# Kernel tuning notes

Hardware: AMD Instinct MI355X
Metric: run time of the kernel (lower is better)

The kernel has to match this reference:

```python
import jax, jax.numpy as jnp
import numpy as np

NUM_NODES = 100000
NFEAT = 128
EMBED_DIM = 128
NHEADS = 2
NHID = EMBED_DIM // NHEADS  # 64
REL_DIM = 128
NUM_REL = 500
E1 = 288000  # 1-hop edges
E2 = 32000   # 2-hop edges
E = E1 + E2
ALPHA = 0.2  # LeakyReLU slope
EPS = 1e-16


def setup_inputs() -> dict:
    key = jax.random.key(0)
    ks = jax.random.split(key, 10)
    edge_index = jax.random.randint(ks[0], (2, E), 0, NUM_NODES, dtype=jnp.int32)
    x = jax.random.normal(ks[1], (NUM_NODES, NFEAT), dtype=jnp.float32)
    r = jax.random.normal(ks[2], (NUM_REL, REL_DIM), dtype=jnp.float32)
    edge_type = jax.random.randint(ks[3], (E1,), 0, NUM_REL, dtype=jnp.int32)
    edge_type_nhop = jax.random.randint(ks[4], (E2, 2), 0, NUM_REL, dtype=jnp.int32)
    # learned params (get_param -> xavier-ish normal)
    s = 0.02
    W_heads = jax.random.normal(ks[5], (NHEADS, 2 * NFEAT + REL_DIM, NHID), dtype=jnp.float32) * s
    a_heads = jax.random.normal(ks[6], (NHEADS, NHID, 1), dtype=jnp.float32) * s
    W_out = jax.random.normal(ks[7], (2 * (NHID * NHEADS) + EMBED_DIM, NHEADS * NHID), dtype=jnp.float32) * s
    a_out = jax.random.normal(ks[8], (NHEADS * NHID, 1), dtype=jnp.float32) * s
    W_r = jax.random.normal(ks[9], (REL_DIM, EMBED_DIM), dtype=jnp.float32) * s
    return {"edge_index": edge_index, "x": x, "r": r, "edge_type": edge_type,
            "edge_type_nhop": edge_type_nhop, "W_heads": W_heads, "a_heads": a_heads,
            "W_out": W_out, "a_out": a_out, "W_r": W_r}


def _gat_layer(edge_index, x, edge_embed, W, a, concat):
    src = edge_index[0]
    dst = edge_index[1]
    # [E, 2*in + rel] -> [E, out]
    edge_h = jnp.concatenate([x[src], x[dst], edge_embed], axis=1) @ W
    e = jax.nn.leaky_relu(jnp.squeeze(edge_h @ a, axis=-1), negative_slope=ALPHA)  # [E]
    # segment softmax over src groups
    seg_max = jax.ops.segment_max(e, src, num_segments=NUM_NODES)
    w = jnp.exp(e - seg_max[src])
    denom = jax.ops.segment_sum(w, src, num_segments=NUM_NODES)
    att = w / (denom[src] + EPS)  # dropout p=0.0 -> identity
    out = jax.ops.segment_sum(att[:, None] * edge_h, src, num_segments=NUM_NODES)  # [N, out]
    return jax.nn.elu(out) if concat else out


def reference(edge_index, x, r, edge_type, edge_type_nhop, W_heads, a_heads, W_out, a_out, W_r):
    # first-pass relation edge embeddings
    edge_embed = jnp.concatenate(
        [r[edge_type], r[edge_type_nhop[:, 0]] + r[edge_type_nhop[:, 1]]], axis=0)  # [E, rel]
    # multi-head attention layers (concat heads)
    heads = [_gat_layer(edge_index, x, edge_embed, W_heads[h], a_heads[h], True)
             for h in range(NHEADS)]
    x1 = jnp.concatenate(heads, axis=1)  # [N, nheads*nhid]; dropout p=0 identity
    # transform relations
    r2 = r @ W_r  # [num_rel, embed_dim]
    edge_embed2 = jnp.concatenate(
        [r2[edge_type], r2[edge_type_nhop[:, 0]] + r2[edge_type_nhop[:, 1]]], axis=0)
    out = jax.nn.elu(_gat_layer(edge_index, x1, edge_embed2, W_out, a_out, False))
    return out, r2
```

## Files before the change

### kernel.cpp

```cpp
#include <hip/hip_runtime.h>
#include <math.h>

#define NNODES 100000
#define NREL 500
#define E1 288000
#define ETOT 320000
#define LALPHA 0.2f
#define SEPS 1e-16f
#define NB_SCAN ((NNODES + 255) / 256)
#define GTILES 6250
#define GTPB 5
#define GGRID (GTILES / GTPB)

typedef __attribute__((ext_vector_type(8))) short bf16x8;
typedef __attribute__((ext_vector_type(4))) float f32x4;

__device__ __forceinline__ unsigned short f2bf(float x) {
  unsigned int u = __float_as_uint(x);
  unsigned int r = (u + 0x7fffu + ((u >> 16) & 1u)) >> 16;
  return (unsigned short)r;
}
__device__ __forceinline__ unsigned int packbf2(float lo, float hi) {
  return (unsigned int)f2bf(lo) | ((unsigned int)f2bf(hi) << 16);
}
__device__ __forceinline__ float unpk_lo(unsigned int u) { return __uint_as_float(u << 16); }
__device__ __forceinline__ float unpk_hi(unsigned int u) {
  return __uint_as_float(u & 0xffff0000u);
}
__device__ __forceinline__ float lrelu(float e) { return (e >= 0.f) ? e : LALPHA * e; }

__device__ __forceinline__ float wave_max64(float v) {
#pragma unroll
  for (int o = 32; o >= 1; o >>= 1) v = fmaxf(v, __shfl_xor(v, o, 64));
  return v;
}
__device__ __forceinline__ float wave_sum64(float v) {
#pragma unroll
  for (int o = 32; o >= 1; o >>= 1) v += __shfl_xor(v, o, 64);
  return v;
}
__device__ __forceinline__ float red16(float v) {
  v += __shfl_xor(v, 1, 64);
  v += __shfl_xor(v, 2, 64);
  v += __shfl_xor(v, 4, 64);
  v += __shfl_xor(v, 8, 64);
  return v;
}

__global__ void k_zero_int(int* __restrict__ p, int n) {
  int i = blockIdx.x * blockDim.x + threadIdx.x;
  if (i < n) p[i] = 0;
}

__global__ void k_count(const int* __restrict__ src, int* __restrict__ cnt) {
  int e = blockIdx.x * blockDim.x + threadIdx.x;
  if (e < ETOT) atomicAdd(&cnt[src[e]], 1);
}

__global__ void k_scan_a(const int* __restrict__ cnt, int* __restrict__ rowstart,
                         int* __restrict__ blockTot) {
  __shared__ int s[256];
  int t = threadIdx.x;
  int idx = blockIdx.x * 256 + t;
  int v = (idx < NNODES) ? cnt[idx] : 0;
  s[t] = v;
  __syncthreads();
  for (int off = 1; off < 256; off <<= 1) {
    int xv = (t >= off) ? s[t - off] : 0;
    __syncthreads();
    s[t] += xv;
    __syncthreads();
  }
  if (idx < NNODES) rowstart[idx] = s[t] - v;
  if (t == 255) blockTot[blockIdx.x] = s[255];
}

__global__ void k_scan_b(const int* __restrict__ blockTot, int* __restrict__ blockOff) {
  __shared__ int s[512];
  int t = threadIdx.x;
  int v = (t < NB_SCAN) ? blockTot[t] : 0;
  s[t] = v;
  __syncthreads();
  for (int off = 1; off < 512; off <<= 1) {
    int xv = (t >= off) ? s[t - off] : 0;
    __syncthreads();
    s[t] += xv;
    __syncthreads();
  }
  if (t < NB_SCAN) blockOff[t] = s[t] - v;
}

__global__ void k_scan_c(int* __restrict__ rowstart, const int* __restrict__ blockOff,
                         int* __restrict__ cursor) {
  int idx = blockIdx.x * 256 + threadIdx.x;
  if (idx < NNODES) {
    int v = rowstart[idx] + blockOff[blockIdx.x];
    rowstart[idx] = v;
    cursor[idx] = v;
  }
  if (idx == 0) rowstart[NNODES] = ETOT;
}

__global__ void k_scatter(const int* __restrict__ src, int* __restrict__ cursor,
                          int* __restrict__ perm) {
  int e = blockIdx.x * blockDim.x + threadIdx.x;
  if (e < ETOT) {
    int pos = atomicAdd(&cursor[src[e]], 1);
    perm[pos] = e;
  }
}

__global__ void k_relprep1(const float* __restrict__ r, const float* __restrict__ Wh,
                           const float* __restrict__ ah, unsigned int* __restrict__ rW1p,
                           float* __restrict__ srel1) {
  __shared__ float vals[128];
  int t = blockIdx.x;
  int tid = threadIdx.x;
  int h = tid >> 6, kk = tid & 63;
  const float* wcol = Wh + h * 24576 + 256 * 64 + kk;
  const float* rrow = r + t * 128;
  float acc = 0.f;
#pragma unroll 4
  for (int d = 0; d < 128; ++d) acc = fmaf(rrow[d], wcol[d * 64], acc);
  vals[tid] = acc;
  float p = wave_sum64(acc * ah[h * 64 + kk]);
  if (kk == 0) srel1[t * 2 + h] = p;
  __syncthreads();
  if (tid < 64) rW1p[t * 64 + tid] = packbf2(vals[2 * tid], vals[2 * tid + 1]);
}

__global__ void k_r2(const float* __restrict__ r, const float* __restrict__ Wr,
                     float* __restrict__ r2out) {
  int t = blockIdx.x;
  int c = threadIdx.x;
  float acc = 0.f;
#pragma unroll 4
  for (int d = 0; d < 128; ++d) acc = fmaf(r[t * 128 + d], Wr[d * 128 + c], acc);
  r2out[t * 128 + c] = acc;
}

__global__ void k_relprep2(const float* __restrict__ r2, const float* __restrict__ Wo,
                           const float* __restrict__ ao, unsigned int* __restrict__ rW2p,
                           float* __restrict__ srel2) {
  __shared__ float s[128];
  __shared__ float vals[128];
  int t = blockIdx.x;
  int k = threadIdx.x;
  float acc = 0.f;
#pragma unroll 4
  for (int d = 0; d < 128; ++d) acc = fmaf(r2[t * 128 + d], Wo[(256 + d) * 128 + k], acc);
  vals[k] = acc;
  s[k] = acc * ao[k];
  __syncthreads();
  for (int off = 64; off >= 1; off >>= 1) {
    if (k < off) s[k] += s[k + off];
    __syncthreads();
  }
  if (k == 0) srel2[t] = s[0];
  if (k < 64) rW2p[t * 64 + k] = packbf2(vals[2 * k], vals[2 * k + 1]);
}

template <int LAYER>
__global__ void k_packb(const float* __restrict__ W, unsigned short* __restrict__ Wb) {
  int c = blockIdx.x;
  int d = threadIdx.x;
  float v;
  if (LAYER == 1) {
    int h = (c >> 6) & 1, part = c >> 7, kc = c & 63;
    v = W[h * 24576 + (part * 128 + d) * 64 + kc];
  } else {
    int part = c >> 7, kc = c & 127;
    v = W[(part * 128 + d) * 128 + kc];
  }
  Wb[c * 128 + d] = f2bf(v);
}

template <int LAYER>
__global__ __launch_bounds__(256) void k_gemm_mfma(const void* __restrict__ Xin,
                                                   const unsigned short* __restrict__ Wb,
                                                   const float* __restrict__ avec,
                                                   unsigned int* __restrict__ xWp,
                                                   float* __restrict__ sc) {
  const int lane = threadIdx.x & 63;
  const int wave = threadIdx.x >> 6;
  const int colv = lane & 15;
  const int kg = lane >> 4;

  bf16x8 b[4][4];
#pragma unroll
  for (int t = 0; t < 4; ++t)
#pragma unroll
    for (int s = 0; s < 4; ++s)
      b[t][s] = *(const bf16x8*)(Wb + (size_t)(wave * 64 + t * 16 + colv) * 128 + s * 32 +
                                 kg * 8);
  float av[4];
#pragma unroll
  for (int t = 0; t < 4; ++t) av[t] = avec[(wave & 1) * 64 + t * 16 + colv];
  const int slot = (LAYER == 1) ? (((wave & 1) << 1) | (wave >> 1)) : wave;

  const float4* xf4 = (const float4*)Xin;
  const uint4* xu4 = (const uint4*)Xin;
  int tile = blockIdx.x * GTPB;

  float4 cf[8];
  uint4 cu[4];
  {
    int ar = tile * 16 + colv;
    if (LAYER == 1) {
      int base = ar * 32 + kg * 2;
#pragma unroll
      for (int s = 0; s < 4; ++s) {
        cf[2 * s] = xf4[base + s * 8];
        cf[2 * s + 1] = xf4[base + s * 8 + 1];
      }
    } else {
      int base = ar * 16 + kg;
#pragma unroll
      for (int s = 0; s < 4; ++s) cu[s] = xu4[base + s * 4];
    }
  }

  for (int it = 0; it < GTPB; ++it, ++tile) {
    float4 nf[8];
    uint4 nu[4];
    const bool hasnext = (it + 1 < GTPB);
    if (hasnext) {
      int ar = (tile + 1) * 16 + colv;
      if (LAYER == 1) {
        int base = ar * 32 + kg * 2;
#pragma unroll
        for (int s = 0; s < 4; ++s) {
          nf[2 * s] = xf4[base + s * 8];
          nf[2 * s + 1] = xf4[base + s * 8 + 1];
        }
      } else {
        int base = ar * 16 + kg;
#pragma unroll
        for (int s = 0; s < 4; ++s) nu[s] = xu4[base + s * 4];
      }
    }

    bf16x8 a[4];
    if (LAYER == 1) {
#pragma unroll
      for (int s = 0; s < 4; ++s) {
        union {
          unsigned short us[8];
          bf16x8 v;
        } u;
        u.us[0] = f2bf(cf[2 * s].x); u.us[1] = f2bf(cf[2 * s].y);
        u.us[2] = f2bf(cf[2 * s].z); u.us[3] = f2bf(cf[2 * s].w);
        u.us[4] = f2bf(cf[2 * s + 1].x); u.us[5] = f2bf(cf[2 * s + 1].y);
        u.us[6] = f2bf(cf[2 * s + 1].z); u.us[7] = f2bf(cf[2 * s + 1].w);
        a[s] = u.v;
      }
    } else {
#pragma unroll
      for (int s = 0; s < 4; ++s) {
        union {
          uint4 q;
          bf16x8 v;
        } u;
        u.q = cu[s];
        a[s] = u.v;
      }
    }

    f32x4 acc[4];
#pragma unroll
    for (int t = 0; t < 4; ++t) acc[t] = (f32x4){0.f, 0.f, 0.f, 0.f};
#pragma unroll
    for (int s = 0; s < 4; ++s)
#pragma unroll
      for (int t = 0; t < 4; ++t)
        acc[t] = __builtin_amdgcn_mfma_f32_16x16x32_bf16(a[s], b[t][s], acc[t], 0, 0, 0);

    const int rbase = tile * 16 + kg * 4;
    const int m = colv >> 1;
    const bool evn = (colv & 1) == 0;
#pragma unroll
    for (int i = 0; i < 4; ++i) {
      unsigned int* orow = xWp + (size_t)(rbase + i) * 128 + wave * 32;
#pragma unroll
      for (int t = 0; t < 4; ++t) {
        float lo = acc[t][i];
        float other = __shfl_xor(lo, 1, 64);
        if (evn) orow[t * 8 + m] = packbf2(lo, other);
      }
      float p = 0.f;
#pragma unroll
      for (int t = 0; t < 4; ++t) p = fmaf(acc[t][i], av[t], p);
      p = red16(p);
      if (colv == 0) sc[(size_t)(rbase + i) * 4 + slot] = p;
    }

    if (hasnext) {
      if (LAYER == 1) {
#pragma unroll
        for (int j = 0; j < 8; ++j) cf[j] = nf[j];
      } else {
#pragma unroll
        for (int j = 0; j < 4; ++j) cu[j] = nu[j];
      }
    }
  }
}

__global__ void k_eprep1(const int* __restrict__ perm, const int* __restrict__ srcA,
                         const int* __restrict__ dstA, const int* __restrict__ et,
                         const int* __restrict__ et2, const float* __restrict__ sc1,
                         const float* __restrict__ srel1, int* __restrict__ srcp,
                         int* __restrict__ dnp, int2* __restrict__ t12,
                         float2* __restrict__ lgp1) {
  int p = blockIdx.x * 256 + threadIdx.x;
  if (p >= ETOT) return;
  int ed = perm[p];
  int src = srcA[ed], dn = dstA[ed];
  int t1, t2 = -1;
  float rel0, rel1;
  if (ed < E1) {
    t1 = et[ed];
    float2 sr = ((const float2*)srel1)[t1];
    rel0 = sr.x;
    rel1 = sr.y;
  } else {
    int2 tt = ((const int2*)et2)[ed - E1];
    t1 = tt.x;
    t2 = tt.y;
    float2 sa = ((const float2*)srel1)[t1];
    float2 sb = ((const float2*)srel1)[t2];
    rel0 = sa.x + sb.x;
    rel1 = sa.y + sb.y;
  }
  float4 ssv = ((const float4*)sc1)[src];
  float4 sdv = ((const float4*)sc1)[dn];
  lgp1[p] = make_float2(lrelu(ssv.x + sdv.y + rel0), lrelu(ssv.z + sdv.w + rel1));
  srcp[p] = src;
  dnp[p] = dn;
  t12[p] = make_int2(t1, t2);
}

__global__ void k_eprep2(const int* __restrict__ srcp, const int* __restrict__ dnp,
                         const int2* __restrict__ t12, const float* __restrict__ sc2,
                         const float* __restrict__ srel2, float* __restrict__ lgp2) {
  int p = blockIdx.x * 256 + threadIdx.x;
  if (p >= ETOT) return;
  int src = srcp[p], dn = dnp[p];
  int2 tt = t12[p];
  float rel = srel2[tt.x];
  if (tt.y >= 0) rel += srel2[tt.y];
  float4 ssv = ((const float4*)sc2)[src];
  float4 sdv = ((const float4*)sc2)[dn];
  lgp2[p] = lrelu((ssv.x + ssv.y) + (sdv.z + sdv.w) + rel);
}

__global__ __launch_bounds__(256) void k_agg1(
    const int* __restrict__ rowstart, const float2* __restrict__ lgp1,
    const int* __restrict__ dnp, const int2* __restrict__ t12,
    const unsigned int* __restrict__ xWp, const unsigned int* __restrict__ rW1p,
    unsigned int* __restrict__ x1b) {
  int n = blockIdx.x * 4 + (threadIdx.x >> 6);
  int lane = threadIdx.x & 63;
  int q = lane & 15, g = lane >> 4;
  int s0 = rowstart[n];
  int deg = rowstart[n + 1] - s0;
  int jj = q + 16 * g;
  float r0 = 0.f, r1 = 0.f;
  if (deg > 0) {
    float m0 = -3.4e38f, m1 = -3.4e38f, d0 = 0.f, d1 = 0.f;
    float ac0[4] = {0.f, 0.f, 0.f, 0.f}, ac1[4] = {0.f, 0.f, 0.f, 0.f};
    for (int base = 0; base < deg; base += 64) {
      int i = base + lane;
      float lg0 = -3.4e38f, lg1 = -3.4e38f;
      int dn = 0;
      int2 tt = make_int2(0, -1);
      if (i < deg) {
        float2 l2 = lgp1[s0 + i];
        lg0 = l2.x;
        lg1 = l2.y;
        dn = dnp[s0 + i];
        tt = t12[s0 + i];
      }
      float nm0 = fmaxf(m0, wave_max64(lg0));
      float nm1 = fmaxf(m1, wave_max64(lg1));
      float rs0 = __expf(m0 - nm0), rs1 = __expf(m1 - nm1);
      float w0 = __expf(lg0 - nm0), w1 = __expf(lg1 - nm1);
      d0 = d0 * rs0 + wave_sum64(w0);
      d1 = d1 * rs1 + wave_sum64(w1);
#pragma unroll
      for (int k = 0; k < 4; ++k) {
        float rs = (k < 2) ? rs0 : rs1;
        ac0[k] *= rs;
        ac1[k] *= rs;
      }
      m0 = nm0;
      m1 = nm1;
      int cnt = min(64, deg - base);
      int steps = (cnt + 3) >> 2;
      for (int s = 0; s < steps; ++s) {
        int e = s * 4 + g;
        float a0 = __shfl(w0, e, 64);
        float a1 = __shfl(w1, e, 64);
        int dne = __shfl(dn, e, 64);
        int t1e = __shfl(tt.x, e, 64);
        int t2e = __shfl(tt.y, e, 64);
        const unsigned int* xr = xWp + (size_t)dne * 128 + 64;
        const unsigned int* rp = rW1p + (size_t)t1e * 64;
#pragma unroll
        for (int k = 0; k < 4; ++k) {
          int j2 = q + 16 * k;
          float as = (k < 2) ? a0 : a1;
          unsigned int ud = xr[j2];
          unsigned int ur = rp[j2];
          float rv0 = unpk_lo(ur), rv1 = unpk_hi(ur);
          if (t2e >= 0) {
            unsigned int u2 = rW1p[(size_t)t2e * 64 + j2];
            rv0 += unpk_lo(u2);
            rv1 += unpk_hi(u2);
          }
          ac0[k] = fmaf(as, unpk_lo(ud) + rv0, ac0[k]);
          ac1[k] = fmaf(as, unpk_hi(ud) + rv1, ac1[k]);
        }
      }
    }
#pragma unroll
    for (int k = 0; k < 4; ++k) {
      ac0[k] += __shfl_xor(ac0[k], 16, 64);
      ac0[k] += __shfl_xor(ac0[k], 32, 64);
      ac1[k] += __shfl_xor(ac1[k], 16, 64);
      ac1[k] += __shfl_xor(ac1[k], 32, 64);
    }
    float a0g = (g == 0) ? ac0[0] : (g == 1) ? ac0[1] : (g == 2) ? ac0[2] : ac0[3];
    float a1g = (g == 0) ? ac1[0] : (g == 1) ? ac1[1] : (g == 2) ? ac1[2] : ac1[3];
    float dsel = (g < 2) ? d0 : d1;
    float isel = 1.f / (dsel + SEPS);
    unsigned int us = xWp[(size_t)n * 128 + jj];
    float o0 = (a0g + dsel * unpk_lo(us)) * isel;
    float o1 = (a1g + dsel * unpk_hi(us)) * isel;
    r0 = (o0 > 0.f) ? o0 : __expf(o0) - 1.f;
    r1 = (o1 > 0.f) ? o1 : __expf(o1) - 1.f;
  }
  x1b[(size_t)n * 64 + jj] = packbf2(r0, r1);
}

__global__ __launch_bounds__(256) void k_agg2(
    const int* __restrict__ rowstart, const float* __restrict__ lgp2,
    const int* __restrict__ dnp, const int2* __restrict__ t12,
    const unsigned int* __restrict__ xWp, const unsigned int* __restrict__ rW2p,
    float* __restrict__ outp) {
  int n = blockIdx.x * 4 + (threadIdx.x >> 6);
  int lane = threadIdx.x & 63;
  int q = lane & 15, g = lane >> 4;
  int s0 = rowstart[n];
  int deg = rowstart[n + 1] - s0;
  int jj = q + 16 * g;
  float r0 = 0.f, r1 = 0.f;
  if (deg > 0) {
    float m = -3.4e38f, d = 0.f;
    float ac0[4] = {0.f, 0.f, 0.f, 0.f}, ac1[4] = {0.f, 0.f, 0.f, 0.f};
    for (int base = 0; base < deg; base += 64) {
      int i = base + lane;
      float lg = -3.4e38f;
      int dn = 0;
      int2 tt = make_int2(0, -1);
      if (i < deg) {
        lg = lgp2[s0 + i];
        dn = dnp[s0 + i];
        tt = t12[s0 + i];
      }
      float nm = fmaxf(m, wave_max64(lg));
      float rs = __expf(m - nm);
      float w = __expf(lg - nm);
      d = d * rs + wave_sum64(w);
#pragma unroll
      for (int k = 0; k < 4; ++k) {
        ac0[k] *= rs;
        ac1[k] *= rs;
      }
      m = nm;
      int cnt = min(64, deg - base);
      int steps = (cnt + 3) >> 2;
      for (int s = 0; s < steps; ++s) {
        int e = s * 4 + g;
        float a = __shfl(w, e, 64);
        int dne = __shfl(dn, e, 64);
        int t1e = __shfl(tt.x, e, 64);
        int t2e = __shfl(tt.y, e, 64);
        const unsigned int* xr = xWp + (size_t)dne * 128 + 64;
        const unsigned int* rp = rW2p + (size_t)t1e * 64;
#pragma unroll
        for (int k = 0; k < 4; ++k) {
          int j2 = q + 16 * k;
          unsigned int ud = xr[j2];
          unsigned int ur = rp[j2];
          float rv0 = unpk_lo(ur), rv1 = unpk_hi(ur);
          if (t2e >= 0) {
            unsigned int u2 = rW2p[(size_t)t2e * 64 + j2];
            rv0 += unpk_lo(u2);
            rv1 += unpk_hi(u2);
          }
          ac0[k] = fmaf(a, unpk_lo(ud) + rv0, ac0[k]);
          ac1[k] = fmaf(a, unpk_hi(ud) + rv1, ac1[k]);
        }
      }
    }
#pragma unroll
    for (int k = 0; k < 4; ++k) {
      ac0[k] += __shfl_xor(ac0[k], 16, 64);
      ac0[k] += __shfl_xor(ac0[k], 32, 64);
      ac1[k] += __shfl_xor(ac1[k], 16, 64);
      ac1[k] += __shfl_xor(ac1[k], 32, 64);
    }
    float a0g = (g == 0) ? ac0[0] : (g == 1) ? ac0[1] : (g == 2) ? ac0[2] : ac0[3];
    float a1g = (g == 0) ? ac1[0] : (g == 1) ? ac1[1] : (g == 2) ? ac1[2] : ac1[3];
    float inv = 1.f / (d + SEPS);
    unsigned int us = xWp[(size_t)n * 128 + jj];
    float o0 = (a0g + d * unpk_lo(us)) * inv;
    float o1 = (a1g + d * unpk_hi(us)) * inv;
    r0 = (o0 > 0.f) ? o0 : __expf(o0) - 1.f;
    r1 = (o1 > 0.f) ? o1 : __expf(o1) - 1.f;
  }
  ((float2*)outp)[(size_t)n * 64 + jj] = make_float2(r0, r1);
}

extern "C" void kernel_launch(void* const* d_in, const int* in_sizes, int n_in, void* d_out,
                              int out_size, void* d_ws, size_t ws_size, hipStream_t stream) {
  const int* edge_index = (const int*)d_in[0];
  const int* srcA = edge_index;
  const int* dstA = edge_index + ETOT;
  const float* x = (const float*)d_in[1];
  const float* r = (const float*)d_in[2];
  const int* et = (const int*)d_in[3];
  const int* et2 = (const int*)d_in[4];
  const float* Wh = (const float*)d_in[5];
  const float* ah = (const float*)d_in[6];
  const float* Wo = (const float*)d_in[7];
  const float* ao = (const float*)d_in[8];
  const float* Wr = (const float*)d_in[9];
  float* out = (float*)d_out;
  float* r2out = out + (size_t)NNODES * 128;

  char* ws = (char*)d_ws;
  size_t o = 0;
  auto alloc = [&](size_t bytes) {
    char* p = ws + o;
    o += (bytes + 255) & ~(size_t)255;
    return p;
  };
  unsigned int* xWp = (unsigned int*)alloc((size_t)NNODES * 128 * 4);
  float* sc1 = (float*)alloc((size_t)NNODES * 4 * 4);
  float* sc2 = (float*)alloc((size_t)NNODES * 4 * 4);
  unsigned int* rW1p = (unsigned int*)alloc((size_t)NREL * 64 * 4);
  float* srel1 = (float*)alloc(2 * NREL * 4);
  unsigned int* rW2p = (unsigned int*)alloc((size_t)NREL * 64 * 4);
  float* srel2 = (float*)alloc(NREL * 4);
  unsigned int* x1b = (unsigned int*)alloc((size_t)NNODES * 64 * 4);
  unsigned short* Wb1 = (unsigned short*)alloc(256 * 128 * 2);
  unsigned short* Wb2 = (unsigned short*)alloc(256 * 128 * 2);
  int* cnt = (int*)alloc(NNODES * 4);
  int* rowstart = (int*)alloc((NNODES + 1) * 4);
  int* cursor = (int*)alloc(NNODES * 4);
  int* blockTot = (int*)alloc(512 * 4);
  int* blockOff = (int*)alloc(512 * 4);
  int* perm = (int*)alloc(ETOT * 4);
  int* srcp = (int*)alloc(ETOT * 4);
  int* dnp = (int*)alloc(ETOT * 4);
  int2* t12 = (int2*)alloc((size_t)ETOT * 8);
  float2* lgp1 = (float2*)alloc((size_t)ETOT * 8);
  float* lgp2 = (float*)alloc(ETOT * 4);

  const int EB = (ETOT + 255) / 256;

  k_zero_int<<<(NNODES + 255) / 256, 256, 0, stream>>>(cnt, NNODES);
  k_count<<<EB, 256, 0, stream>>>(srcA, cnt);
  k_scan_a<<<NB_SCAN, 256, 0, stream>>>(cnt, rowstart, blockTot);
  k_scan_b<<<1, 512, 0, stream>>>(blockTot, blockOff);
  k_scan_c<<<NB_SCAN, 256, 0, stream>>>(rowstart, blockOff, cursor);
  k_scatter<<<EB, 256, 0, stream>>>(srcA, cursor, perm);

  k_relprep1<<<NREL, 128, 0, stream>>>(r, Wh, ah, rW1p, srel1);
  k_r2<<<NREL, 128, 0, stream>>>(r, Wr, r2out);
  k_relprep2<<<NREL, 128, 0, stream>>>(r2out, Wo, ao, rW2p, srel2);
  k_packb<1><<<256, 128, 0, stream>>>(Wh, Wb1);
  k_packb<2><<<256, 128, 0, stream>>>(Wo, Wb2);

  k_gemm_mfma<1><<<GGRID, 256, 0, stream>>>(x, Wb1, ah, xWp, sc1);
  k_eprep1<<<EB, 256, 0, stream>>>(perm, srcA, dstA, et, et2, sc1, srel1, srcp, dnp, t12,
                                   lgp1);
  k_agg1<<<NNODES / 4, 256, 0, stream>>>(rowstart, lgp1, dnp, t12, xWp, rW1p, x1b);

  k_gemm_mfma<2><<<GGRID, 256, 0, stream>>>(x1b, Wb2, ao, xWp, sc2);
  k_eprep2<<<EB, 256, 0, stream>>>(srcp, dnp, t12, sc2, srel2, lgp2);
  k_agg2<<<NNODES / 4, 256, 0, stream>>>(rowstart, lgp2, dnp, t12, xWp, rW2p, out);
}
```

Measured before the change: 402.9 us.

## Drop segment-max softmax, precompute clamped exp weights and atomic denominators in eprep

The aggregation kernels no longer do an online segment max and rescale. Instead the edge-prep kernels compute exp of the clamped logit directly and accumulate per-source denominators with atomics, and the aggregation kernels read precomputed weights per edge group without shuffles. The relation prep kernels are fused into one, as are the two weight-pack kernels, which cuts launches. The cost is giving up max-subtraction for numerical safety, with a clamp at 60 as the only guard, and taking on float atomic contention and nondeterministic summation order.

```diff
diff --git a/kernel.cpp b/kernel.cpp
--- a/kernel.cpp
+++ b/kernel.cpp
@@ -28,12 +28,8 @@
   return __uint_as_float(u & 0xffff0000u);
 }
 __device__ __forceinline__ float lrelu(float e) { return (e >= 0.f) ? e : LALPHA * e; }
-
-__device__ __forceinline__ float wave_max64(float v) {
-#pragma unroll
-  for (int o = 32; o >= 1; o >>= 1) v = fmaxf(v, __shfl_xor(v, o, 64));
-  return v;
-}
+__device__ __forceinline__ float wexp(float lg) { return __expf(fminf(lg, 60.f)); }
+
 __device__ __forceinline__ float wave_sum64(float v) {
 #pragma unroll
   for (int o = 32; o >= 1; o >>= 1) v += __shfl_xor(v, o, 64);
@@ -129,26 +125,24 @@
   if (tid < 64) rW1p[t * 64 + tid] = packbf2(vals[2 * tid], vals[2 * tid + 1]);
 }
 
-__global__ void k_r2(const float* __restrict__ r, const float* __restrict__ Wr,
-                     float* __restrict__ r2out) {
-  int t = blockIdx.x;
-  int c = threadIdx.x;
-  float acc = 0.f;
-#pragma unroll 4
-  for (int d = 0; d < 128; ++d) acc = fmaf(r[t * 128 + d], Wr[d * 128 + c], acc);
-  r2out[t * 128 + c] = acc;
-}
-
-__global__ void k_relprep2(const float* __restrict__ r2, const float* __restrict__ Wo,
-                           const float* __restrict__ ao, unsigned int* __restrict__ rW2p,
-                           float* __restrict__ srel2) {
+__global__ void k_relprep2f(const float* __restrict__ r, const float* __restrict__ Wr,
+                            const float* __restrict__ Wo, const float* __restrict__ ao,
+                            unsigned int* __restrict__ rW2p, float* __restrict__ srel2,
+                            float* __restrict__ r2out) {
+  __shared__ float v2[128];
   __shared__ float s[128];
   __shared__ float vals[128];
   int t = blockIdx.x;
   int k = threadIdx.x;
+  float a2 = 0.f;
+#pragma unroll 4
+  for (int d = 0; d < 128; ++d) a2 = fmaf(r[t * 128 + d], Wr[d * 128 + k], a2);
+  r2out[t * 128 + k] = a2;
+  v2[k] = a2;
+  __syncthreads();
   float acc = 0.f;
 #pragma unroll 4
-  for (int d = 0; d < 128; ++d) acc = fmaf(r2[t * 128 + d], Wo[(256 + d) * 128 + k], acc);
+  for (int d = 0; d < 128; ++d) acc = fmaf(v2[d], Wo[(256 + d) * 128 + k], acc);
   vals[k] = acc;
   s[k] = acc * ao[k];
   __syncthreads();
@@ -160,19 +154,19 @@
   if (k < 64) rW2p[t * 64 + k] = packbf2(vals[2 * k], vals[2 * k + 1]);
 }
 
-template <int LAYER>
-__global__ void k_packb(const float* __restrict__ W, unsigned short* __restrict__ Wb) {
-  int c = blockIdx.x;
+__global__ void k_packb_both(const float* __restrict__ Wh, const float* __restrict__ Wo,
+                             unsigned short* __restrict__ Wb1,
+                             unsigned short* __restrict__ Wb2) {
+  int c = blockIdx.x & 255;
+  int layer = blockIdx.x >> 8;
   int d = threadIdx.x;
-  float v;
-  if (LAYER == 1) {
+  if (layer == 0) {
     int h = (c >> 6) & 1, part = c >> 7, kc = c & 63;
-    v = W[h * 24576 + (part * 128 + d) * 64 + kc];
+    Wb1[c * 128 + d] = f2bf(Wh[h * 24576 + (part * 128 + d) * 64 + kc]);
   } else {
     int part = c >> 7, kc = c & 127;
-    v = W[(part * 128 + d) * 128 + kc];
-  }
-  Wb[c * 128 + d] = f2bf(v);
+    Wb2[c * 128 + d] = f2bf(Wo[(part * 128 + d) * 128 + kc]);
+  }
 }
 
 template <int LAYER>
@@ -311,7 +305,7 @@
                          const int* __restrict__ et2, const float* __restrict__ sc1,
                          const float* __restrict__ srel1, int* __restrict__ srcp,
                          int* __restrict__ dnp, int2* __restrict__ t12,
-                         float2* __restrict__ lgp1) {
+                         float2* __restrict__ wexp1, float* __restrict__ denom1) {
   int p = blockIdx.x * 256 + threadIdx.x;
   if (p >= ETOT) return;
   int ed = perm[p];
@@ -334,7 +328,11 @@
   }
   float4 ssv = ((const float4*)sc1)[src];
   float4 sdv = ((const float4*)sc1)[dn];
-  lgp1[p] = make_float2(lrelu(ssv.x + sdv.y + rel0), lrelu(ssv.z + sdv.w + rel1));
+  float w0 = wexp(lrelu(ssv.x + sdv.y + rel0));
+  float w1 = wexp(lrelu(ssv.z + sdv.w + rel1));
+  wexp1[p] = make_float2(w0, w1);
+  atomicAdd(&denom1[2 * src], w0);
+  atomicAdd(&denom1[2 * src + 1], w1);
   srcp[p] = src;
   dnp[p] = dn;
   t12[p] = make_int2(t1, t2);
@@ -342,7 +340,8 @@
 
 __global__ void k_eprep2(const int* __restrict__ srcp, const int* __restrict__ dnp,
                          const int2* __restrict__ t12, const float* __restrict__ sc2,
-                         const float* __restrict__ srel2, float* __restrict__ lgp2) {
+                         const float* __restrict__ srel2, float* __restrict__ wexp2,
+                         float* __restrict__ denom2) {
   int p = blockIdx.x * 256 + threadIdx.x;
   if (p >= ETOT) return;
   int src = srcp[p], dn = dnp[p];
@@ -351,14 +350,16 @@
   if (tt.y >= 0) rel += srel2[tt.y];
   float4 ssv = ((const float4*)sc2)[src];
   float4 sdv = ((const float4*)sc2)[dn];
-  lgp2[p] = lrelu((ssv.x + ssv.y) + (sdv.z + sdv.w) + rel);
+  float w = wexp(lrelu((ssv.x + ssv.y) + (sdv.z + sdv.w) + rel));
+  wexp2[p] = w;
+  atomicAdd(&denom2[src], w);
 }
 
 __global__ __launch_bounds__(256) void k_agg1(
-    const int* __restrict__ rowstart, const float2* __restrict__ lgp1,
+    const int* __restrict__ rowstart, const float2* __restrict__ wexp1,
     const int* __restrict__ dnp, const int2* __restrict__ t12,
     const unsigned int* __restrict__ xWp, const unsigned int* __restrict__ rW1p,
-    unsigned int* __restrict__ x1b) {
+    const float2* __restrict__ denom1, unsigned int* __restrict__ x1b) {
   int n = blockIdx.x * 4 + (threadIdx.x >> 6);
   int lane = threadIdx.x & 63;
   int q = lane & 15, g = lane >> 4;
@@ -367,60 +368,37 @@
   int jj = q + 16 * g;
   float r0 = 0.f, r1 = 0.f;
   if (deg > 0) {
-    float m0 = -3.4e38f, m1 = -3.4e38f, d0 = 0.f, d1 = 0.f;
     float ac0[4] = {0.f, 0.f, 0.f, 0.f}, ac1[4] = {0.f, 0.f, 0.f, 0.f};
-    for (int base = 0; base < deg; base += 64) {
-      int i = base + lane;
-      float lg0 = -3.4e38f, lg1 = -3.4e38f;
-      int dn = 0;
-      int2 tt = make_int2(0, -1);
-      if (i < deg) {
-        float2 l2 = lgp1[s0 + i];
-        lg0 = l2.x;
-        lg1 = l2.y;
-        dn = dnp[s0 + i];
-        tt = t12[s0 + i];
-      }
-      float nm0 = fmaxf(m0, wave_max64(lg0));
-      float nm1 = fmaxf(m1, wave_max64(lg1));
-      float rs0 = __expf(m0 - nm0), rs1 = __expf(m1 - nm1);
-      float w0 = __expf(lg0 - nm0), w1 = __expf(lg1 - nm1);
-      d0 = d0 * rs0 + wave_sum64(w0);
-      d1 = d1 * rs1 + wave_sum64(w1);
+    const int pend = s0 + deg;
+    for (int p0 = s0; p0 < pend; p0 += 4) {
+      int p = p0 + g;
+      float w0 = 0.f, w1 = 0.f;
+      int dne = 0, t1e = 0, t2e = -1;
+      if (p < pend) {
+        float2 wv = wexp1[p];
+        w0 = wv.x;
+        w1 = wv.y;
+        dne = dnp[p];
+        int2 tt = t12[p];
+        t1e = tt.x;
+        t2e = tt.y;
+      }
+      const unsigned int* xr = xWp + (size_t)dne * 128 + 64;
+      const unsigned int* rp = rW1p + (size_t)t1e * 64;
 #pragma unroll
       for (int k = 0; k < 4; ++k) {
-        float rs = (k < 2) ? rs0 : rs1;
-        ac0[k] *= rs;
-        ac1[k] *= rs;
-      }
-      m0 = nm0;
-      m1 = nm1;
-      int cnt = min(64, deg - base);
-      int steps = (cnt + 3) >> 2;
-      for (int s = 0; s < steps; ++s) {
-        int e = s * 4 + g;
-        float a0 = __shfl(w0, e, 64);
-        float a1 = __shfl(w1, e, 64);
-        int dne = __shfl(dn, e, 64);
-        int t1e = __shfl(tt.x, e, 64);
-        int t2e = __shfl(tt.y, e, 64);
-        const unsigned int* xr = xWp + (size_t)dne * 128 + 64;
-        const unsigned int* rp = rW1p + (size_t)t1e * 64;
-#pragma unroll
-        for (int k = 0; k < 4; ++k) {
-          int j2 = q + 16 * k;
-          float as = (k < 2) ? a0 : a1;
-          unsigned int ud = xr[j2];
-          unsigned int ur = rp[j2];
-          float rv0 = unpk_lo(ur), rv1 = unpk_hi(ur);
-          if (t2e >= 0) {
-            unsigned int u2 = rW1p[(size_t)t2e * 64 + j2];
-            rv0 += unpk_lo(u2);
-            rv1 += unpk_hi(u2);
-          }
-          ac0[k] = fmaf(as, unpk_lo(ud) + rv0, ac0[k]);
-          ac1[k] = fmaf(as, unpk_hi(ud) + rv1, ac1[k]);
+        int j2 = q + 16 * k;
+        float as = (k < 2) ? w0 : w1;
+        unsigned int ud = xr[j2];
+        unsigned int ur = rp[j2];
+        float rv0 = unpk_lo(ur), rv1 = unpk_hi(ur);
+        if (t2e >= 0) {
+          unsigned int u2 = rW1p[(size_t)t2e * 64 + j2];
+          rv0 += unpk_lo(u2);
+          rv1 += unpk_hi(u2);
         }
+        ac0[k] = fmaf(as, unpk_lo(ud) + rv0, ac0[k]);
+        ac1[k] = fmaf(as, unpk_hi(ud) + rv1, ac1[k]);
       }
     }
 #pragma unroll
@@ -432,7 +410,8 @@
     }
     float a0g = (g == 0) ? ac0[0] : (g == 1) ? ac0[1] : (g == 2) ? ac0[2] : ac0[3];
     float a1g = (g == 0) ? ac1[0] : (g == 1) ? ac1[1] : (g == 2) ? ac1[2] : ac1[3];
-    float dsel = (g < 2) ? d0 : d1;
+    float2 dd = denom1[n];
+    float dsel = (g < 2) ? dd.x : dd.y;
     float isel = 1.f / (dsel + SEPS);
     unsigned int us = xWp[(size_t)n * 128 + jj];
     float o0 = (a0g + dsel * unpk_lo(us)) * isel;
@@ -444,10 +423,10 @@
 }
 
 __global__ __launch_bounds__(256) void k_agg2(
-    const int* __restrict__ rowstart, const float* __restrict__ lgp2,
+    const int* __restrict__ rowstart, const float* __restrict__ wexp2,
     const int* __restrict__ dnp, const int2* __restrict__ t12,
     const unsigned int* __restrict__ xWp, const unsigned int* __restrict__ rW2p,
-    float* __restrict__ outp) {
+    const float* __restrict__ denom2, float* __restrict__ outp) {
   int n = blockIdx.x * 4 + (threadIdx.x >> 6);
   int lane = threadIdx.x & 63;
   int q = lane & 15, g = lane >> 4;
@@ -456,52 +435,34 @@
   int jj = q + 16 * g;
   float r0 = 0.f, r1 = 0.f;
   if (deg > 0) {
-    float m = -3.4e38f, d = 0.f;
     float ac0[4] = {0.f, 0.f, 0.f, 0.f}, ac1[4] = {0.f, 0.f, 0.f, 0.f};
-    for (int base = 0; base < deg; base += 64) {
-      int i = base + lane;
-      float lg = -3.4e38f;
-      int dn = 0;
-      int2 tt = make_int2(0, -1);
-      if (i < deg) {
-        lg = lgp2[s0 + i];
-        dn = dnp[s0 + i];
-        tt = t12[s0 + i];
-      }
-      float nm = fmaxf(m, wave_max64(lg));
-      float rs = __expf(m - nm);
-      float w = __expf(lg - nm);
-      d = d * rs + wave_sum64(w);
+    const int pend = s0 + deg;
+    for (int p0 = s0; p0 < pend; p0 += 4) {
+      int p = p0 + g;
+      float w = 0.f;
+      int dne = 0, t1e = 0, t2e = -1;
+      if (p < pend) {
+        w = wexp2[p];
+        dne = dnp[p];
+        int2 tt = t12[p];
+        t1e = tt.x;
+        t2e = tt.y;
+      }
+      const unsigned int* xr = xWp + (size_t)dne * 128 + 64;
+      const unsigned int* rp = rW2p + (size_t)t1e * 64;
 #pragma unroll
       for (int k = 0; k < 4; ++k) {
-        ac0[k] *= rs;
-        ac1[k] *= rs;
-      }
-      m = nm;
-      int cnt = min(64, deg - base);
-      int steps = (cnt + 3) >> 2;
-      for (int s = 0; s < steps; ++s) {
-        int e = s * 4 + g;
-        float a = __shfl(w, e, 64);
-        int dne = __shfl(dn, e, 64);
-        int t1e = __shfl(tt.x, e, 64);
-        int t2e = __shfl(tt.y, e, 64);
-        const unsigned int* xr = xWp + (size_t)dne * 128 + 64;
-        const unsigned int* rp = rW2p + (size_t)t1e * 64;
-#pragma unroll
-        for (int k = 0; k < 4; ++k) {
-          int j2 = q + 16 * k;
-          unsigned int ud = xr[j2];
-          unsigned int ur = rp[j2];
-          float rv0 = unpk_lo(ur), rv1 = unpk_hi(ur);
-          if (t2e >= 0) {
-            unsigned int u2 = rW2p[(size_t)t2e * 64 + j2];
-            rv0 += unpk_lo(u2);
-            rv1 += unpk_hi(u2);
-          }
-          ac0[k] = fmaf(a, unpk_lo(ud) + rv0, ac0[k]);
-          ac1[k] = fmaf(a, unpk_hi(ud) + rv1, ac1[k]);
+        int j2 = q + 16 * k;
+        unsigned int ud = xr[j2];
+        unsigned int ur = rp[j2];
+        float rv0 = unpk_lo(ur), rv1 = unpk_hi(ur);
+        if (t2e >= 0) {
+          unsigned int u2 = rW2p[(size_t)t2e * 64 + j2];
+          rv0 += unpk_lo(u2);
+          rv1 += unpk_hi(u2);
         }
+        ac0[k] = fmaf(w, unpk_lo(ud) + rv0, ac0[k]);
+        ac1[k] = fmaf(w, unpk_hi(ud) + rv1, ac1[k]);
       }
     }
 #pragma unroll
@@ -513,6 +474,7 @@
     }
     float a0g = (g == 0) ? ac0[0] : (g == 1) ? ac0[1] : (g == 2) ? ac0[2] : ac0[3];
     float a1g = (g == 0) ? ac1[0] : (g == 1) ? ac1[1] : (g == 2) ? ac1[2] : ac1[3];
+    float d = denom2[n];
     float inv = 1.f / (d + SEPS);
     unsigned int us = xWp[(size_t)n * 128 + jj];
     float o0 = (a0g + d * unpk_lo(us)) * inv;
@@ -550,6 +512,10 @@
   unsigned int* xWp = (unsigned int*)alloc((size_t)NNODES * 128 * 4);
   float* sc1 = (float*)alloc((size_t)NNODES * 4 * 4);
   float* sc2 = (float*)alloc((size_t)NNODES * 4 * 4);
+  int* zb = (int*)alloc((size_t)4 * NNODES * 4);
+  int* cnt = zb;
+  float* denom1 = (float*)(zb + NNODES);
+  float* denom2 = (float*)(zb + 3 * NNODES);
   unsigned int* rW1p = (unsigned int*)alloc((size_t)NREL * 64 * 4);
   float* srel1 = (float*)alloc(2 * NREL * 4);
   unsigned int* rW2p = (unsigned int*)alloc((size_t)NREL * 64 * 4);
@@ -557,7 +523,6 @@
   unsigned int* x1b = (unsigned int*)alloc((size_t)NNODES * 64 * 4);
   unsigned short* Wb1 = (unsigned short*)alloc(256 * 128 * 2);
   unsigned short* Wb2 = (unsigned short*)alloc(256 * 128 * 2);
-  int* cnt = (int*)alloc(NNODES * 4);
   int* rowstart = (int*)alloc((NNODES + 1) * 4);
   int* cursor = (int*)alloc(NNODES * 4);
   int* blockTot = (int*)alloc(512 * 4);
@@ -566,12 +531,13 @@
   int* srcp = (int*)alloc(ETOT * 4);
   int* dnp = (int*)alloc(ETOT * 4);
   int2* t12 = (int2*)alloc((size_t)ETOT * 8);
-  float2* lgp1 = (float2*)alloc((size_t)ETOT * 8);
-  float* lgp2 = (float*)alloc(ETOT * 4);
+  float2* wexp1 = (float2*)alloc((size_t)ETOT * 8);
+  float* wexp2 = (float*)alloc(ETOT * 4);
 
   const int EB = (ETOT + 255) / 256;
 
-  k_zero_int<<<(NNODES + 255) / 256, 256, 0, stream>>>(cnt, NNODES);
+  k_zero_int<<<(4 * NNODES + 255) / 256, 256, 0, stream>>>(zb, 4 * NNODES);
+
   k_count<<<EB, 256, 0, stream>>>(srcA, cnt);
   k_scan_a<<<NB_SCAN, 256, 0, stream>>>(cnt, rowstart, blockTot);
   k_scan_b<<<1, 512, 0, stream>>>(blockTot, blockOff);
@@ -579,17 +545,16 @@
   k_scatter<<<EB, 256, 0, stream>>>(srcA, cursor, perm);
 
   k_relprep1<<<NREL, 128, 0, stream>>>(r, Wh, ah, rW1p, srel1);
-  k_r2<<<NREL, 128, 0, stream>>>(r, Wr, r2out);
-  k_relprep2<<<NREL, 128, 0, stream>>>(r2out, Wo, ao, rW2p, srel2);
-  k_packb<1><<<256, 128, 0, stream>>>(Wh, Wb1);
-  k_packb<2><<<256, 128, 0, stream>>>(Wo, Wb2);
+  k_relprep2f<<<NREL, 128, 0, stream>>>(r, Wr, Wo, ao, rW2p, srel2, r2out);
+  k_packb_both<<<512, 128, 0, stream>>>(Wh, Wo, Wb1, Wb2);
 
   k_gemm_mfma<1><<<GGRID, 256, 0, stream>>>(x, Wb1, ah, xWp, sc1);
   k_eprep1<<<EB, 256, 0, stream>>>(perm, srcA, dstA, et, et2, sc1, srel1, srcp, dnp, t12,
-                                   lgp1);
-  k_agg1<<<NNODES / 4, 256, 0, stream>>>(rowstart, lgp1, dnp, t12, xWp, rW1p, x1b);
+                                   wexp1, denom1);
+  k_agg1<<<NNODES / 4, 256, 0, stream>>>(rowstart, wexp1, dnp, t12, xWp, rW1p,
+                                         (const float2*)denom1, x1b);
 
   k_gemm_mfma<2><<<GGRID, 256, 0, stream>>>(x1b, Wb2, ao, xWp, sc2);
-  k_eprep2<<<EB, 256, 0, stream>>>(srcp, dnp, t12, sc2, srel2, lgp2);
-  k_agg2<<<NNODES / 4, 256, 0, stream>>>(rowstart, lgp2, dnp, t12, xWp, rW2p, out);
-}
+  k_eprep2<<<EB, 256, 0, stream>>>(srcp, dnp, t12, sc2, srel2, wexp2, denom2);
+  k_agg2<<<NNODES / 4, 256, 0, stream>>>(rowstart, wexp2, dnp, t12, xWp, rW2p, denom2, out);
+}
```

After: 428.0 us. 1.06x slower.
